# Kernel tuning notes

Measured on AMD Instinct MI355X. Metric: run time of the kernel, lower is better.

Reference implementation:

```python
import jax, jax.numpy as jnp
import numpy as np

B, N, C_IN, C_OUT = 4, 1024, 64, 64


def setup_inputs() -> dict:
    key = jax.random.key(0)
    k_x, k_adj, k0, k1, k2, k_b = jax.random.split(key, 6)
    x = jax.random.normal(k_x, (B, N, C_IN), dtype=jnp.float32)
    adj = jax.random.uniform(k_adj, (B, N, N), dtype=jnp.float32)  # unused by forward, kept for API fidelity
    s = 1.0 / np.sqrt(C_IN)  # torch nn.Linear kaiming-uniform range
    W0 = jax.random.uniform(k0, (C_OUT, C_IN), dtype=jnp.float32, minval=-s, maxval=s)
    W1 = jax.random.uniform(k1, (C_OUT, C_IN), dtype=jnp.float32, minval=-s, maxval=s)
    W2 = jax.random.uniform(k2, (C_OUT, C_IN), dtype=jnp.float32, minval=-s, maxval=s)
    bias = jax.random.uniform(k_b, (C_OUT, 1), dtype=jnp.float32)  # reset_parameters: uniform_ on learnable bias
    return {"x": x, "adj": adj, "W0": W0, "W1": W1, "W2": W2, "bias": bias}


def reference(x, adj, W0, W1, W2, bias):
    # Original: expand x to O(N^2) basis tensors (columns, rows, global-sum) and
    # apply a separate bias-free Linear to each, then sum + bias.
    # Algebraic identity: linear(broadcast(x)) == broadcast(linear(x)), so we do
    # the three GEMMs at O(N) cost and only broadcast/sum at O(N^2 * C_out).
    y_cols = jnp.einsum('bnc,oc->bno', x, W0)           # L0(X_columns): varies along j
    y_rows = jnp.einsum('bnc,oc->bno', x, W1)           # L1(X_rows):    varies along i
    y_sum = jnp.einsum('bc,oc->bo', x.sum(axis=1), W2)  # L2(X_sum):     global per-batch
    # out[b, i, j, o] = y_cols[b, j, o] + y_rows[b, i, o] + y_sum[b, o] + bias[o]
    out = (y_cols[:, None, :, :]
           + y_rows[:, :, None, :]
           + y_sum[:, None, None, :]
           + bias[:, 0])
    return out
```

## Files before the change

kernel.cpp:

```cpp
#include <hip/hip_runtime.h>

#define NB 4
#define NN 1024
#define CC 64
#define BPB (NN / 4)
#define IT 4

typedef float f4_native __attribute__((ext_vector_type(4)));

__global__ void k_gemm(const float* __restrict__ x, const float* __restrict__ W0,
                       const float* __restrict__ W1,
                       float* __restrict__ yc, float* __restrict__ yr,
                       float* __restrict__ partials) {
    __shared__ float sW0[64][65];
    __shared__ float sW1[64][65];
    __shared__ float sX[4][64];
    const int t = threadIdx.x;
    const int b = blockIdx.x / BPB;
    const int n0 = (blockIdx.x % BPB) * 4;
    for (int idx = t; idx < 64 * 64; idx += 256) {
        sW0[idx >> 6][idx & 63] = W0[idx];
        sW1[idx >> 6][idx & 63] = W1[idx];
    }
    const int o = t & 63, r = t >> 6;
    sX[r][o] = x[((size_t)(b * NN + n0 + r)) * CC + o];
    __syncthreads();
    float a0 = 0.f, a1 = 0.f;
    #pragma unroll
    for (int c = 0; c < 64; ++c) {
        const float xv = sX[r][c];
        a0 += xv * sW0[o][c];
        a1 += xv * sW1[o][c];
    }
    const size_t oidx = ((size_t)(b * NN + n0 + r)) * CC + o;
    yc[oidx] = a0;
    yr[oidx] = a1;
    if (r == 0)
        partials[(size_t)blockIdx.x * 64 + o] =
            sX[0][o] + sX[1][o] + sX[2][o] + sX[3][o];
}

__global__ void k_ysb(const float* __restrict__ partials, const float* __restrict__ W2,
                      const float* __restrict__ bias, float* __restrict__ ysb) {
    const int b = blockIdx.x;
    const int t = threadIdx.x;
    const int c = t & 63, g = t >> 6;
    __shared__ float sPart[4][64];
    __shared__ float sXsum[64];
    float acc = 0.f;
    const float* pb = partials + (size_t)b * BPB * 64;
    for (int blk = g; blk < BPB; blk += 4)
        acc += pb[blk * 64 + c];
    sPart[g][c] = acc;
    __syncthreads();
    if (t < 64)
        sXsum[t] = sPart[0][t] + sPart[1][t] + sPart[2][t] + sPart[3][t];
    __syncthreads();
    if (t < 64) {
        float v = bias[t];
        const float* w = W2 + t * CC;
        #pragma unroll 8
        for (int cc = 0; cc < CC; ++cc) v += sXsum[cc] * w[cc];
        ysb[b * CC + t] = v;
    }
}

__global__ void k_bcast(const float4* __restrict__ yc4, const float4* __restrict__ yr4,
                        const float4* __restrict__ ysb4, float4* __restrict__ out4) {
    const int t  = threadIdx.x;
    const int o4 = t & 15;
    const int j0 = t >> 4;
    const int b  = blockIdx.x / (NN / IT);
    const int i0 = (blockIdx.x % (NN / IT)) * IT;
    const float4 ys = ysb4[b * 16 + o4];
    float4 yrr[IT];
    #pragma unroll
    for (int r = 0; r < IT; ++r) {
        float4 v = yr4[(size_t)(b * NN + i0 + r) * 16 + o4];
        yrr[r].x = v.x + ys.x; yrr[r].y = v.y + ys.y;
        yrr[r].z = v.z + ys.z; yrr[r].w = v.w + ys.w;
    }
    const float4* ycb = yc4 + (size_t)b * NN * 16;
    float4* ob = out4 + (size_t)(b * NN + i0) * (NN * 16);
    #pragma unroll 2
    for (int j = j0; j < NN; j += 16) {
        float4 v = ycb[j * 16 + o4];
        #pragma unroll
        for (int r = 0; r < IT; ++r) {
            float4 w;
            w.x = v.x + yrr[r].x; w.y = v.y + yrr[r].y;
            w.z = v.z + yrr[r].z; w.w = v.w + yrr[r].w;
            __builtin_nontemporal_store(*(const f4_native*)&w,
                                        (f4_native*)&ob[(size_t)r * (NN * 16) + j * 16 + o4]);
        }
    }
}

extern "C" void kernel_launch(void* const* d_in, const int* in_sizes, int n_in,
                              void* d_out, int out_size, void* d_ws, size_t ws_size,
                              hipStream_t stream) {
    const float* x    = (const float*)d_in[0];
    const float* W0   = (const float*)d_in[2];
    const float* W1   = (const float*)d_in[3];
    const float* W2   = (const float*)d_in[4];
    const float* bias = (const float*)d_in[5];
    float* out = (float*)d_out;

    float* ws       = (float*)d_ws;
    float* ysb      = ws;
    float* yc       = ws + 256;
    float* yr       = yc + NB * NN * CC;
    float* partials = yr + NB * NN * CC;

    k_gemm<<<NB * BPB, 256, 0, stream>>>(x, W0, W1, yc, yr, partials);
    k_ysb<<<NB, 256, 0, stream>>>(partials, W2, bias, ysb);
    k_bcast<<<NB * (NN / IT), 256, 0, stream>>>((const float4*)yc, (const float4*)yr,
                                                (const float4*)ysb, (float4*)out);
}
```

Before: 239.8 us.

## Retile broadcast kernel: hold y_cols tile in registers, stage y_rows in LDS

The broadcast kernel now assigns each block a 256-column by 32-row tile. The y_cols slice for the tile is loaded once into 16 float4 registers per thread, and the 32 y_rows vectors, with y_sum and bias already added, are staged in shared memory. Each thread then streams nontemporal stores over the 32 rows. This cuts repeated reloads of y_cols per output row and gives each thread more consecutive stores. The cost is higher register pressure, a block barrier, and a different grid shape for a kernel that is bound by output writes.

```diff
diff --git a/kernel.cpp b/kernel.cpp
--- a/kernel.cpp
+++ b/kernel.cpp
@@ -4,7 +4,8 @@
 #define NN 1024
 #define CC 64
 #define BPB (NN / 4)
-#define IT 4
+#define JC 256
+#define IC 32
 
 typedef float f4_native __attribute__((ext_vector_type(4)));
 
@@ -67,31 +68,41 @@
 
 __global__ void k_bcast(const float4* __restrict__ yc4, const float4* __restrict__ yr4,
                         const float4* __restrict__ ysb4, float4* __restrict__ out4) {
+    __shared__ float4 sYr[IC][16];
     const int t  = threadIdx.x;
     const int o4 = t & 15;
-    const int j0 = t >> 4;
-    const int b  = blockIdx.x / (NN / IT);
-    const int i0 = (blockIdx.x % (NN / IT)) * IT;
-    const float4 ys = ysb4[b * 16 + o4];
-    float4 yrr[IT];
+    const int bpb = (NN / JC) * (NN / IC);
+    const int b   = blockIdx.x / bpb;
+    const int rem = blockIdx.x % bpb;
+    const int j0  = (rem / (NN / IC)) * JC;
+    const int i0  = (rem % (NN / IC)) * IC;
+
+    float4 ycreg[16];
+    const float4* ycb = yc4 + ((size_t)b * NN + j0) * 16;
     #pragma unroll
-    for (int r = 0; r < IT; ++r) {
-        float4 v = yr4[(size_t)(b * NN + i0 + r) * 16 + o4];
-        yrr[r].x = v.x + ys.x; yrr[r].y = v.y + ys.y;
-        yrr[r].z = v.z + ys.z; yrr[r].w = v.w + ys.w;
+    for (int s = 0; s < 16; ++s)
+        ycreg[s] = ycb[s * 256 + t];
+
+    const float4* yrb = yr4 + ((size_t)b * NN + i0) * 16;
+    for (int idx = t; idx < IC * 16; idx += 256) {
+        float4 v = yrb[idx];
+        float4 ysv = ysb4[b * 16 + (idx & 15)];
+        v.x += ysv.x; v.y += ysv.y; v.z += ysv.z; v.w += ysv.w;
+        sYr[idx >> 4][idx & 15] = v;
     }
-    const float4* ycb = yc4 + (size_t)b * NN * 16;
-    float4* ob = out4 + (size_t)(b * NN + i0) * (NN * 16);
-    #pragma unroll 2
-    for (int j = j0; j < NN; j += 16) {
-        float4 v = ycb[j * 16 + o4];
+    __syncthreads();
+
+    float4* ob = out4 + (((size_t)b * NN + i0) * NN + j0) * 16;
+    for (int i = 0; i < IC; ++i) {
+        const float4 yrv = sYr[i][o4];
+        float4* obi = ob + (size_t)i * (NN * 16);
         #pragma unroll
-        for (int r = 0; r < IT; ++r) {
+        for (int s = 0; s < 16; ++s) {
             float4 w;
-            w.x = v.x + yrr[r].x; w.y = v.y + yrr[r].y;
-            w.z = v.z + yrr[r].z; w.w = v.w + yrr[r].w;
+            w.x = ycreg[s].x + yrv.x; w.y = ycreg[s].y + yrv.y;
+            w.z = ycreg[s].z + yrv.z; w.w = ycreg[s].w + yrv.w;
             __builtin_nontemporal_store(*(const f4_native*)&w,
-                                        (f4_native*)&ob[(size_t)r * (NN * 16) + j * 16 + o4]);
+                                        (f4_native*)&obi[s * 256 + t]);
         }
     }
 }
@@ -114,6 +125,6 @@
 
     k_gemm<<<NB * BPB, 256, 0, stream>>>(x, W0, W1, yc, yr, partials);
     k_ysb<<<NB, 256, 0, stream>>>(partials, W2, bias, ysb);
-    k_bcast<<<NB * (NN / IT), 256, 0, stream>>>((const float4*)yc, (const float4*)yr,
-                                                (const float4*)ysb, (float4*)out);
+    k_bcast<<<NB * (NN / JC) * (NN / IC), 256, 0, stream>>>(
+        (const float4*)yc, (const float4*)yr, (const float4*)ysb, (float4*)out);
 }
```

Measured after the change: 231.0 us. -3.7%, faster.
